# Performance work log

Hardware: AMD Instinct MI355X
Metric: run time of the kernel (lower is better)

Reference implementation:

```python
import jax, jax.numpy as jnp
import numpy as np

D = 2048  # dims
T = 8192  # sequence length


def _layernorm(x, g, b):
    m = jnp.mean(x, axis=-1, keepdims=True)
    v = jnp.mean(jnp.square(x - m), axis=-1, keepdims=True)
    return (x - m) * jax.lax.rsqrt(v + 1e-5) * g + b


def _lerp(a, b, t):
    # torch.lerp(a, b, t) = a + t*(b-a)
    return a + t * (b - a)


def _wkv(k, v, time_first, time_decay):
    """RWKV power-decay attention (numerically stable scan).
    k, v: [T, D]. w = -exp(time_decay) is the per-channel log-decay."""
    u = time_first
    w = -jnp.exp(time_decay)

    def step(carry, kv):
        aa, bb, pp = carry  # running num, den, max-exponent, each [D]
        kt, vt = kv
        ww = u + kt
        p = jnp.maximum(pp, ww)
        e1 = jnp.exp(pp - p)
        e2 = jnp.exp(ww - p)
        out = (e1 * aa + e2 * vt) / (e1 * bb + e2)
        ww2 = pp + w
        p2 = jnp.maximum(ww2, kt)
        e1 = jnp.exp(ww2 - p2)
        e2 = jnp.exp(kt - p2)
        return (e1 * aa + e2 * vt, e1 * bb + e2, p2), out

    init = (jnp.zeros((D,), k.dtype), jnp.zeros((D,), k.dtype),
            jnp.full((D,), -1e38, k.dtype))
    _, out = jax.lax.scan(step, init, (k, v))
    return out  # [T, D]


def setup_inputs() -> dict:
    key = jax.random.key(0)
    ks = iter(jax.random.split(key, 40))
    s = 1.0 / np.sqrt(D)
    inp = {"x": jax.random.normal(next(ks), (T, D), jnp.float32)}
    for name in ["attk", "attv", "attr", "atto", "ffnk", "ffnv", "ffnr"]:
        inp[name + "_w"] = jax.random.normal(next(ks), (D, D), jnp.float32) * s
        inp[name + "_b"] = jax.random.normal(next(ks), (D,), jnp.float32) * 0.02
    inp["ln1_g"] = jnp.ones((D,), jnp.float32)
    inp["ln1_b"] = jnp.zeros((D,), jnp.float32)
    inp["ln2_g"] = jnp.ones((D,), jnp.float32)
    inp["ln2_b"] = jnp.zeros((D,), jnp.float32)
    for name in ["attmixk", "attmixv", "attmixr", "ffnmixk", "ffnmixr"]:
        inp[name] = jax.random.uniform(next(ks), (D,), jnp.float32)
    inp["time_first"] = jax.random.normal(next(ks), (D,), jnp.float32) * 0.1
    inp["time_decay"] = jax.random.normal(next(ks), (D,), jnp.float32) * 0.1
    return inp


def reference(x, attk_w, attk_b, attv_w, attv_b, attr_w, attr_b, atto_w, atto_b,
              ffnk_w, ffnk_b, ffnv_w, ffnv_b, ffnr_w, ffnr_b,
              ln1_g, ln1_b, ln2_g, ln2_b,
              attmixk, attmixv, attmixr, ffnmixk, ffnmixr,
              time_first, time_decay):
    # --- time-mix (attention) branch ---
    xy = _layernorm(x, ln1_g, ln1_b)
    tc = jnp.roll(xy, 1, axis=0)  # token shift
    k = _lerp(tc, xy, attmixk) @ attk_w.T + attk_b
    v = _lerp(tc, xy, attmixv) @ attv_w.T + attv_b
    r = jax.nn.sigmoid(_lerp(tc, xy, attmixr) @ attr_w.T + attr_b)
    wkv = _wkv(k, v, time_first, time_decay) * r
    rz = x + wkv @ atto_w.T + atto_b
    # --- channel-mix (FFN) branch ---
    ddd = _layernorm(rz, ln2_g, ln2_b)
    rc = jnp.roll(ddd, 1, axis=0)
    rf = jax.nn.sigmoid(_lerp(rc, ddd, ffnmixr) @ ffnr_w.T + ffnr_b)
    kf = jax.nn.relu(_lerp(rc, ddd, ffnmixk) @ ffnk_w.T + ffnk_b)
    rvm = jnp.square(kf) @ ffnv_w.T + ffnv_b
    return rvm * rf + rz
```

## Files before the change

### kernel.cpp

```cpp
#include <hip/hip_runtime.h>
#include <cstdint>
#include <cstddef>


#define SEQ 8192
#define DIM 2048
#define NCH 128
#define CL  64

typedef unsigned short u16;
typedef __attribute__((ext_vector_type(8))) short bf16x8;
typedef __attribute__((ext_vector_type(4))) float f32x4;

__device__ __forceinline__ u16 f2bf(float f) {
  unsigned x = __float_as_uint(f);
  x += 0x7fffu + ((x >> 16) & 1u);
  return (u16)(x >> 16);
}
__device__ __forceinline__ float bf2f(u16 h) {
  return __uint_as_float((unsigned)h << 16);
}

__global__ void __launch_bounds__(256) convert_weights(
    const float* w0, const float* w1, const float* w2, const float* w3,
    const float* w4, const float* w5, const float* w6, u16* dst)
{
  const float* s;
  switch (blockIdx.y) {
    case 0: s = w0; break; case 1: s = w1; break; case 2: s = w2; break;
    case 3: s = w3; break; case 4: s = w4; break; case 5: s = w5; break;
    default: s = w6; break;
  }
  size_t i = ((size_t)blockIdx.x * 256 + threadIdx.x) * 4;
  float4 f = *(const float4*)(s + i);
  *(ushort4*)(dst + (size_t)blockIdx.y * DIM * DIM + i) =
      make_ushort4(f2bf(f.x), f2bf(f.y), f2bf(f.z), f2bf(f.w));
}

__device__ __forceinline__ void store_mix8(u16* dst, const float* mix,
                                           const float* yc, const float* yp)
{
  float4 ma = *(const float4*)(mix);
  float4 mb = *(const float4*)(mix + 4);
  float mv[8] = {ma.x, ma.y, ma.z, ma.w, mb.x, mb.y, mb.z, mb.w};
  u16 uu[8];
  #pragma unroll
  for (int j = 0; j < 8; ++j)
    uu[j] = f2bf(yp[j] + mv[j] * (yc[j] - yp[j]));
  *(ushort4*)dst       = make_ushort4(uu[0], uu[1], uu[2], uu[3]);
  *(ushort4*)(dst + 4) = make_ushort4(uu[4], uu[5], uu[6], uu[7]);
}

template<int NOUT>
__global__ void __launch_bounds__(256) ln_mix_kernel(
    const float* __restrict__ X, const float* __restrict__ gw, const float* __restrict__ bw,
    const float* __restrict__ mix0, const float* __restrict__ mix1, const float* __restrict__ mix2,
    u16* __restrict__ o0, u16* __restrict__ o1, u16* __restrict__ o2)
{
  const int t  = blockIdx.x;
  const int tp = (t == 0) ? (SEQ - 1) : (t - 1);
  const int tid = threadIdx.x, lane = tid & 63, wid = tid >> 6;
  const int base = tid * 8;
  const float* xc = X + (size_t)t  * DIM + base;
  const float* xp = X + (size_t)tp * DIM + base;
  float4 ca = *(const float4*)xc, cb2 = *(const float4*)(xc + 4);
  float4 pa = *(const float4*)xp, pb2 = *(const float4*)(xp + 4);
  float cv[8] = {ca.x, ca.y, ca.z, ca.w, cb2.x, cb2.y, cb2.z, cb2.w};
  float pv[8] = {pa.x, pa.y, pa.z, pa.w, pb2.x, pb2.y, pb2.z, pb2.w};
  float4 s = {0.f, 0.f, 0.f, 0.f};
  #pragma unroll
  for (int j = 0; j < 8; ++j) {
    s.x += cv[j]; s.y += cv[j] * cv[j];
    s.z += pv[j]; s.w += pv[j] * pv[j];
  }
  #pragma unroll
  for (int off = 32; off > 0; off >>= 1) {
    s.x += __shfl_down(s.x, off);
    s.y += __shfl_down(s.y, off);
    s.z += __shfl_down(s.z, off);
    s.w += __shfl_down(s.w, off);
  }
  __shared__ float4 wred[4];
  if (lane == 0) wred[wid] = s;
  __syncthreads();
  float4 tt;
  tt.x = wred[0].x + wred[1].x + wred[2].x + wred[3].x;
  tt.y = wred[0].y + wred[1].y + wred[2].y + wred[3].y;
  tt.z = wred[0].z + wred[1].z + wred[2].z + wred[3].z;
  tt.w = wred[0].w + wred[1].w + wred[2].w + wred[3].w;
  constexpr float inv = 1.0f / DIM;
  const float mc = tt.x * inv, vc = tt.y * inv - mc * mc;
  const float rc = 1.0f / sqrtf(vc + 1e-5f);
  const float mp = tt.z * inv, vp = tt.w * inv - mp * mp;
  const float rp = 1.0f / sqrtf(vp + 1e-5f);
  float4 ga = *(const float4*)(gw + base), gb = *(const float4*)(gw + base + 4);
  float4 ba = *(const float4*)(bw + base), bb = *(const float4*)(bw + base + 4);
  float gv[8] = {ga.x, ga.y, ga.z, ga.w, gb.x, gb.y, gb.z, gb.w};
  float bv[8] = {ba.x, ba.y, ba.z, ba.w, bb.x, bb.y, bb.z, bb.w};
  float yc[8], yp[8];
  #pragma unroll
  for (int j = 0; j < 8; ++j) {
    yc[j] = (cv[j] - mc) * rc * gv[j] + bv[j];
    yp[j] = (pv[j] - mp) * rp * gv[j] + bv[j];
  }
  store_mix8(o0 + (size_t)t * DIM + base, mix0 + base, yc, yp);
  store_mix8(o1 + (size_t)t * DIM + base, mix1 + base, yc, yp);
  if constexpr (NOUT == 3)
    store_mix8(o2 + (size_t)t * DIM + base, mix2 + base, yc, yp);
}

template<int EPI>
__global__ void __launch_bounds__(256, 4) gemm_bt(
    const u16* __restrict__ A, const u16* __restrict__ B,
    const float* __restrict__ bias,
    const float* __restrict__ exf, const u16* __restrict__ exb,
    float* __restrict__ Cf, u16* __restrict__ Cb)
{
  constexpr int BK = 32;
  constexpr int NT = DIM / BK;
  __shared__ u16 As[2][128 * BK];
  __shared__ u16 Bs[2][128 * BK];
  const int tid  = threadIdx.x;
  const int lane = tid & 63;
  const int wid  = tid >> 6;
  const int wr = wid >> 1, wc = wid & 1;
  const int bid = blockIdx.y * gridDim.x + blockIdx.x;
  const int nb  = (bid & 7) * 128 + (bid >> 3);
  const int tn  = (nb & 15) * 128;
  const int tm  = (nb >> 4) * 128;
  const int frow = lane & 15, fko = (lane >> 4) * 8;
  const int cb = wid * 2;
  f32x4 acc[4][4] = {};

#define GSTAGE(b, k0)                                                           \
  {                                                                             \
    _Pragma("unroll")                                                           \
    for (int j = 0; j < 2; ++j) {                                               \
      const int chunk = (cb + j) * 64 + lane;                                   \
      const int row = chunk >> 2;                                               \
      const int c8  = (chunk & 3) * 8;                                          \
      const u16* ga = A + (size_t)(tm + row) * DIM + (k0) + c8;                 \
      const u16* gb = B + (size_t)(tn + row) * DIM + (k0) + c8;                 \
      __builtin_amdgcn_global_load_lds(                                         \
          (const __attribute__((address_space(1))) void*)ga,                    \
          (__attribute__((address_space(3))) void*)(&As[b][0] + (cb + j) * 512),\
          16, 0, 0);                                                            \
      __builtin_amdgcn_global_load_lds(                                         \
          (const __attribute__((address_space(1))) void*)gb,                    \
          (__attribute__((address_space(3))) void*)(&Bs[b][0] + (cb + j) * 512),\
          16, 0, 0);                                                            \
    }                                                                           \
  }

#define GCOMPUTE(b)                                                             \
  {                                                                             \
    bf16x8 af[4], bfr[4];                                                       \
    _Pragma("unroll")                                                           \
    for (int m = 0; m < 4; ++m)                                                 \
      af[m] = *(const bf16x8*)(&As[b][0] + (wr * 64 + m * 16 + frow) * BK + fko);\
    _Pragma("unroll")                                                           \
    for (int n = 0; n < 4; ++n)                                                 \
      bfr[n] = *(const bf16x8*)(&Bs[b][0] + (wc * 64 + n * 16 + frow) * BK + fko);\
    _Pragma("unroll")                                                           \
    for (int m = 0; m < 4; ++m)                                                 \
      _Pragma("unroll")                                                         \
      for (int n = 0; n < 4; ++n)                                               \
        acc[m][n] = __builtin_amdgcn_mfma_f32_16x16x32_bf16(af[m], bfr[n],      \
                                                            acc[m][n], 0, 0, 0);\
  }

  GSTAGE(0, 0);
  __syncthreads();
  #pragma unroll 1
  for (int t = 0; t < NT; t += 2) {
    GSTAGE(1, (t + 1) * BK);
    GCOMPUTE(0);
    __syncthreads();
    if (t + 2 < NT) GSTAGE(0, (t + 2) * BK);
    GCOMPUTE(1);
    __syncthreads();
  }
#undef GSTAGE
#undef GCOMPUTE

  #pragma unroll
  for (int n = 0; n < 4; ++n) {
    const int cn = tn + wc * 64 + n * 16 + frow;
    const float bv = bias[cn];
    #pragma unroll
    for (int m = 0; m < 4; ++m) {
      const int r0 = tm + wr * 64 + m * 16 + (lane >> 4) * 4;
      #pragma unroll
      for (int i = 0; i < 4; ++i) {
        const size_t idx = (size_t)(r0 + i) * DIM + cn;
        float val = acc[m][n][i] + bv;
        if constexpr (EPI == 0)      { Cb[idx] = f2bf(val); }
        else if constexpr (EPI == 1) { Cb[idx] = f2bf(1.0f / (1.0f + __expf(-val))); }
        else if constexpr (EPI == 2) { Cf[idx] = val + exf[idx]; }
        else if constexpr (EPI == 3) { float r = fmaxf(val, 0.0f); Cb[idx] = f2bf(r * r); }
        else                         { Cf[idx] = val * bf2f(exb[idx]) + exf[idx]; }
      }
    }
  }
}

__global__ void __launch_bounds__(256) wkv_phase1(
    const u16* __restrict__ k, const u16* __restrict__ v,
    const float* __restrict__ tdec,
    float* __restrict__ Sa, float* __restrict__ Sb, float* __restrict__ Sp)
{
  const int d = blockIdx.y * 256 + threadIdx.x;
  const int c = blockIdx.x;
  const float w = -__expf(tdec[d]);
  float aa = 0.f, bb = 0.f, pp = -1e38f;
  const int t0 = c * CL;
  for (int t = t0; t < t0 + CL; ++t) {
    const size_t idx = (size_t)t * DIM + d;
    const float kk = bf2f(k[idx]), vv = bf2f(v[idx]);
    const float ww2 = pp + w;
    const float p2 = fmaxf(ww2, kk);
    const float e1 = __expf(ww2 - p2), e2 = __expf(kk - p2);
    aa = e1 * aa + e2 * vv;
    bb = e1 * bb + e2;
    pp = p2;
  }
  Sa[(size_t)c * DIM + d] = aa;
  Sb[(size_t)c * DIM + d] = bb;
  Sp[(size_t)c * DIM + d] = pp;
}

__global__ void __launch_bounds__(256) wkv_phase2(
    const float* __restrict__ Sa, const float* __restrict__ Sb, const float* __restrict__ Sp,
    const float* __restrict__ tdec,
    float* __restrict__ Pa, float* __restrict__ Pb, float* __restrict__ Pp)
{
  const int d = blockIdx.x * 256 + threadIdx.x;
  const float w = -__expf(tdec[d]);
  const float Lw = (float)CL * w;
  float aa = 0.f, bb = 0.f, pp = -1e38f;
  for (int c = 0; c < NCH; ++c) {
    const size_t idx = (size_t)c * DIM + d;
    Pa[idx] = aa; Pb[idx] = bb; Pp[idx] = pp;
    const float dp = pp + Lw;
    const float sa = Sa[idx], sb = Sb[idx], sp = Sp[idx];
    const float p = fmaxf(dp, sp);
    const float e1 = __expf(dp - p), e2 = __expf(sp - p);
    aa = e1 * aa + e2 * sa;
    bb = e1 * bb + e2 * sb;
    pp = p;
  }
}

__global__ void __launch_bounds__(256) wkv_phase3(
    const u16* __restrict__ k, const u16* __restrict__ v, const u16* __restrict__ r,
    const float* __restrict__ Pa, const float* __restrict__ Pb, const float* __restrict__ Pp,
    const float* __restrict__ tfirst, const float* __restrict__ tdec,
    u16* __restrict__ outb)
{
  const int d = blockIdx.y * 256 + threadIdx.x;
  const int c = blockIdx.x;
  const float u = tfirst[d];
  const float w = -__expf(tdec[d]);
  const size_t sidx = (size_t)c * DIM + d;
  float aa = Pa[sidx], bb = Pb[sidx], pp = Pp[sidx];
  const int t0 = c * CL;
  for (int t = t0; t < t0 + CL; ++t) {
    const size_t idx = (size_t)t * DIM + d;
    const float kk = bf2f(k[idx]), vv = bf2f(v[idx]);
    const float ww = u + kk;
    const float p = fmaxf(pp, ww);
    float e1 = __expf(pp - p), e2 = __expf(ww - p);
    const float out = (e1 * aa + e2 * vv) / (e1 * bb + e2);
    outb[idx] = f2bf(out * bf2f(r[idx]));
    const float ww2 = pp + w;
    const float p2 = fmaxf(ww2, kk);
    e1 = __expf(ww2 - p2); e2 = __expf(kk - p2);
    aa = e1 * aa + e2 * vv;
    bb = e1 * bb + e2;
    pp = p2;
  }
}

extern "C" void kernel_launch(void* const* d_in, const int* in_sizes, int n_in,
                              void* d_out, int out_size, void* d_ws, size_t ws_size,
                              hipStream_t stream)
{
  const float* x      = (const float*)d_in[0];
  const float* attk_w = (const float*)d_in[1];
  const float* attk_b = (const float*)d_in[2];
  const float* attv_w = (const float*)d_in[3];
  const float* attv_b = (const float*)d_in[4];
  const float* attr_w = (const float*)d_in[5];
  const float* attr_b = (const float*)d_in[6];
  const float* atto_w = (const float*)d_in[7];
  const float* atto_b = (const float*)d_in[8];
  const float* ffnk_w = (const float*)d_in[9];
  const float* ffnk_b = (const float*)d_in[10];
  const float* ffnv_w = (const float*)d_in[11];
  const float* ffnv_b = (const float*)d_in[12];
  const float* ffnr_w = (const float*)d_in[13];
  const float* ffnr_b = (const float*)d_in[14];
  const float* ln1_g  = (const float*)d_in[15];
  const float* ln1_b  = (const float*)d_in[16];
  const float* ln2_g  = (const float*)d_in[17];
  const float* ln2_b  = (const float*)d_in[18];
  const float* amixk  = (const float*)d_in[19];
  const float* amixv  = (const float*)d_in[20];
  const float* amixr  = (const float*)d_in[21];
  const float* fmixk  = (const float*)d_in[22];
  const float* fmixr  = (const float*)d_in[23];
  const float* tfirst = (const float*)d_in[24];
  const float* tdecay = (const float*)d_in[25];
  float* out = (float*)d_out;

  const size_t WE = (size_t)DIM * DIM;
  const size_t SD = (size_t)SEQ * DIM;
  u16* Wbf = (u16*)d_ws;
  u16* xk  = Wbf + 7 * WE;
  u16* xv  = xk + SD;
  u16* xr  = xv + SD;
  u16* kb  = xr + SD;
  u16* vb  = kb + SD;
  u16* rb  = vb + SD;
  float* Sa = (float*)(rb + SD);
  float* Sb = Sa + (size_t)NCH * DIM;
  float* Sp = Sb + (size_t)NCH * DIM;
  float* Pa = Sp + (size_t)NCH * DIM;
  float* Pb = Pa + (size_t)NCH * DIM;
  float* Pp = Pb + (size_t)NCH * DIM;
  u16*   wkvr = xk;
  float* rz   = (float*)xv;
  u16*   xkf  = kb;
  u16*   xrf  = vb;
  u16*   rf   = rb;
  u16*   kf2  = xk;

  const dim3 gg(DIM / 128, SEQ / 128);
  const dim3 gwkv(NCH, DIM / 256);

  convert_weights<<<dim3(DIM * DIM / 1024, 7), 256, 0, stream>>>(
      attk_w, attv_w, attr_w, atto_w, ffnk_w, ffnv_w, ffnr_w, Wbf);

  ln_mix_kernel<3><<<SEQ, 256, 0, stream>>>(x, ln1_g, ln1_b, amixk, amixv, amixr, xk, xv, xr);
  gemm_bt<0><<<gg, 256, 0, stream>>>(xk, Wbf + 0 * WE, attk_b, nullptr, nullptr, nullptr, kb);
  gemm_bt<0><<<gg, 256, 0, stream>>>(xv, Wbf + 1 * WE, attv_b, nullptr, nullptr, nullptr, vb);
  gemm_bt<1><<<gg, 256, 0, stream>>>(xr, Wbf + 2 * WE, attr_b, nullptr, nullptr, nullptr, rb);
  wkv_phase1<<<gwkv, 256, 0, stream>>>(kb, vb, tdecay, Sa, Sb, Sp);
  wkv_phase2<<<DIM / 256, 256, 0, stream>>>(Sa, Sb, Sp, tdecay, Pa, Pb, Pp);
  wkv_phase3<<<gwkv, 256, 0, stream>>>(kb, vb, rb, Pa, Pb, Pp, tfirst, tdecay, wkvr);
  gemm_bt<2><<<gg, 256, 0, stream>>>(wkvr, Wbf + 3 * WE, atto_b, x, nullptr, rz, nullptr);

  ln_mix_kernel<2><<<SEQ, 256, 0, stream>>>(rz, ln2_g, ln2_b, fmixk, fmixr, nullptr, xkf, xrf, nullptr);
  gemm_bt<1><<<gg, 256, 0, stream>>>(xrf, Wbf + 6 * WE, ffnr_b, nullptr, nullptr, nullptr, rf);
  gemm_bt<3><<<gg, 256, 0, stream>>>(xkf, Wbf + 4 * WE, ffnk_b, nullptr, nullptr, nullptr, kf2);
  gemm_bt<4><<<gg, 256, 0, stream>>>(kf2, Wbf + 5 * WE, ffnv_b, rz, rf, out, nullptr);
}
```

Measured before the change: 1.006 ms.

## Use 256x256 GEMM tiles with 4-stage LDS pipeline and swizzled layout

Rewrites the bf16 GEMM to use 256x256 output tiles computed by 512 threads (8 waves, 128x64 per wave), with a 4-buffer LDS ring prefetching three k-steps ahead and gated by vmcnt waits. The LDS layout is XOR-swizzled to reduce bank conflicts on fragment reads, and MFMA sections get raised wave priority. The larger tile is meant to raise arithmetic intensity and hide global-load latency. In exchange it uses much more LDS (128KB) and registers, and launches only 256 blocks, which may leave CUs underused or lower occupancy.

After: 1.124 ms. 1.12x slower.

```diff
diff --git a/kernel.cpp b/kernel.cpp
--- a/kernel.cpp
+++ b/kernel.cpp
@@ -110,7 +110,7 @@
 }
 
 template<int EPI>
-__global__ void __launch_bounds__(256, 4) gemm_bt(
+__global__ void __launch_bounds__(512, 2) gemm_bt(
     const u16* __restrict__ A, const u16* __restrict__ B,
     const float* __restrict__ bias,
     const float* __restrict__ exf, const u16* __restrict__ exb,
@@ -118,78 +118,103 @@
 {
   constexpr int BK = 32;
   constexpr int NT = DIM / BK;
-  __shared__ u16 As[2][128 * BK];
-  __shared__ u16 Bs[2][128 * BK];
+  __shared__ u16 As[4][256 * BK];
+  __shared__ u16 Bs[4][256 * BK];
   const int tid  = threadIdx.x;
   const int lane = tid & 63;
   const int wid  = tid >> 6;
-  const int wr = wid >> 1, wc = wid & 1;
-  const int bid = blockIdx.y * gridDim.x + blockIdx.x;
-  const int nb  = (bid & 7) * 128 + (bid >> 3);
-  const int tn  = (nb & 15) * 128;
-  const int tm  = (nb >> 4) * 128;
-  const int frow = lane & 15, fko = (lane >> 4) * 8;
-  const int cb = wid * 2;
-  f32x4 acc[4][4] = {};
-
-#define GSTAGE(b, k0)                                                           \
+  const int wr   = wid >> 2;
+  const int wc   = wid & 3;
+  const int bid = blockIdx.x;
+  const int nb  = (bid & 7) * 32 + (bid >> 3);
+  const int tm  = (nb >> 3) * 256;
+  const int tn  = (nb & 7) * 256;
+  const int frow = lane & 15;
+  const int fkc  = lane >> 4;
+
+  f32x4 acc[8][4] = {};
+
+#define STAGE(b, kt)                                                            \
   {                                                                             \
+    const int k0 = (kt) * BK;                                                   \
     _Pragma("unroll")                                                           \
     for (int j = 0; j < 2; ++j) {                                               \
-      const int chunk = (cb + j) * 64 + lane;                                   \
-      const int row = chunk >> 2;                                               \
-      const int c8  = (chunk & 3) * 8;                                          \
-      const u16* ga = A + (size_t)(tm + row) * DIM + (k0) + c8;                 \
-      const u16* gb = B + (size_t)(tn + row) * DIM + (k0) + c8;                 \
+      const int p   = (j * 512 + tid) * 16;                                     \
+      const int q   = p ^ (((p >> 7) & 3) << 4);                                \
+      const int row = q >> 6;                                                   \
+      const int ce  = (q & 63) >> 1;                                            \
       __builtin_amdgcn_global_load_lds(                                         \
-          (const __attribute__((address_space(1))) void*)ga,                    \
-          (__attribute__((address_space(3))) void*)(&As[b][0] + (cb + j) * 512),\
-          16, 0, 0);                                                            \
-      __builtin_amdgcn_global_load_lds(                                         \
-          (const __attribute__((address_space(1))) void*)gb,                    \
-          (__attribute__((address_space(3))) void*)(&Bs[b][0] + (cb + j) * 512),\
+          (const __attribute__((address_space(1))) void*)                       \
+              (A + (size_t)(tm + row) * DIM + k0 + ce),                         \
+          (__attribute__((address_space(3))) void*)((char*)&As[b][0] + p),      \
           16, 0, 0);                                                            \
     }                                                                           \
-  }
-
-#define GCOMPUTE(b)                                                             \
+    _Pragma("unroll")                                                           \
+    for (int j = 0; j < 2; ++j) {                                               \
+      const int p   = (j * 512 + tid) * 16;                                     \
+      const int q   = p ^ (((p >> 7) & 3) << 4);                                \
+      const int row = q >> 6;                                                   \
+      const int ce  = (q & 63) >> 1;                                            \
+      __builtin_amdgcn_global_load_lds(                                         \
+          (const __attribute__((address_space(1))) void*)                       \
+              (B + (size_t)(tn + row) * DIM + k0 + ce),                         \
+          (__attribute__((address_space(3))) void*)((char*)&Bs[b][0] + p),      \
+          16, 0, 0);                                                            \
+    }                                                                           \
+  }
+
+#define COMPUTE(b)                                                              \
   {                                                                             \
-    bf16x8 af[4], bfr[4];                                                       \
-    _Pragma("unroll")                                                           \
-    for (int m = 0; m < 4; ++m)                                                 \
-      af[m] = *(const bf16x8*)(&As[b][0] + (wr * 64 + m * 16 + frow) * BK + fko);\
-    _Pragma("unroll")                                                           \
-    for (int n = 0; n < 4; ++n)                                                 \
-      bfr[n] = *(const bf16x8*)(&Bs[b][0] + (wc * 64 + n * 16 + frow) * BK + fko);\
-    _Pragma("unroll")                                                           \
-    for (int m = 0; m < 4; ++m)                                                 \
+    bf16x8 af[8], bfr[4];                                                       \
+    _Pragma("unroll")                                                           \
+    for (int m = 0; m < 8; ++m) {                                               \
+      const int row = wr * 128 + m * 16 + frow;                                 \
+      const int off = row * 64 + ((fkc ^ ((row >> 1) & 3)) * 16);               \
+      af[m] = *(const bf16x8*)((const char*)&As[b][0] + off);                   \
+    }                                                                           \
+    _Pragma("unroll")                                                           \
+    for (int n = 0; n < 4; ++n) {                                               \
+      const int row = wc * 64 + n * 16 + frow;                                  \
+      const int off = row * 64 + ((fkc ^ ((row >> 1) & 3)) * 16);               \
+      bfr[n] = *(const bf16x8*)((const char*)&Bs[b][0] + off);                  \
+    }                                                                           \
+    __builtin_amdgcn_s_setprio(1);                                              \
+    _Pragma("unroll")                                                           \
+    for (int m = 0; m < 8; ++m)                                                 \
       _Pragma("unroll")                                                         \
       for (int n = 0; n < 4; ++n)                                               \
         acc[m][n] = __builtin_amdgcn_mfma_f32_16x16x32_bf16(af[m], bfr[n],      \
                                                             acc[m][n], 0, 0, 0);\
-  }
-
-  GSTAGE(0, 0);
-  __syncthreads();
+    __builtin_amdgcn_s_setprio(0);                                              \
+  }
+
+  STAGE(0, 0); STAGE(1, 1); STAGE(2, 2);
   #pragma unroll 1
-  for (int t = 0; t < NT; t += 2) {
-    GSTAGE(1, (t + 1) * BK);
-    GCOMPUTE(0);
-    __syncthreads();
-    if (t + 2 < NT) GSTAGE(0, (t + 2) * BK);
-    GCOMPUTE(1);
-    __syncthreads();
-  }
-#undef GSTAGE
-#undef GCOMPUTE
+  for (int t = 0; t < NT - 2; ++t) {
+    asm volatile("s_waitcnt vmcnt(8)" ::: "memory");
+    __builtin_amdgcn_s_barrier();
+    __builtin_amdgcn_sched_barrier(0);
+    if (t < NT - 3) STAGE((t + 3) & 3, t + 3);
+    COMPUTE(t & 3);
+  }
+  asm volatile("s_waitcnt vmcnt(4)" ::: "memory");
+  __builtin_amdgcn_s_barrier();
+  __builtin_amdgcn_sched_barrier(0);
+  COMPUTE((NT - 2) & 3);
+  asm volatile("s_waitcnt vmcnt(0)" ::: "memory");
+  __builtin_amdgcn_s_barrier();
+  __builtin_amdgcn_sched_barrier(0);
+  COMPUTE((NT - 1) & 3);
+#undef STAGE
+#undef COMPUTE
 
   #pragma unroll
   for (int n = 0; n < 4; ++n) {
     const int cn = tn + wc * 64 + n * 16 + frow;
     const float bv = bias[cn];
     #pragma unroll
-    for (int m = 0; m < 4; ++m) {
-      const int r0 = tm + wr * 64 + m * 16 + (lane >> 4) * 4;
+    for (int m = 0; m < 8; ++m) {
+      const int r0 = tm + wr * 128 + m * 16 + (lane >> 4) * 4;
       #pragma unroll
       for (int i = 0; i < 4; ++i) {
         const size_t idx = (size_t)(r0 + i) * DIM + cn;
@@ -335,23 +360,23 @@
   u16*   rf   = rb;
   u16*   kf2  = xk;
 
-  const dim3 gg(DIM / 128, SEQ / 128);
+  const dim3 gg(256);
   const dim3 gwkv(NCH, DIM / 256);
 
   convert_weights<<<dim3(DIM * DIM / 1024, 7), 256, 0, stream>>>(
       attk_w, attv_w, attr_w, atto_w, ffnk_w, ffnv_w, ffnr_w, Wbf);
 
   ln_mix_kernel<3><<<SEQ, 256, 0, stream>>>(x, ln1_g, ln1_b, amixk, amixv, amixr, xk, xv, xr);
-  gemm_bt<0><<<gg, 256, 0, stream>>>(xk, Wbf + 0 * WE, attk_b, nullptr, nullptr, nullptr, kb);
-  gemm_bt<0><<<gg, 256, 0, stream>>>(xv, Wbf + 1 * WE, attv_b, nullptr, nullptr, nullptr, vb);
-  gemm_bt<1><<<gg, 256, 0, stream>>>(xr, Wbf + 2 * WE, attr_b, nullptr, nullptr, nullptr, rb);
+  gemm_bt<0><<<gg, 512, 0, stream>>>(xk, Wbf + 0 * WE, attk_b, nullptr, nullptr, nullptr, kb);
+  gemm_bt<0><<<gg, 512, 0, stream>>>(xv, Wbf + 1 * WE, attv_b, nullptr, nullptr, nullptr, vb);
+  gemm_bt<1><<<gg, 512, 0, stream>>>(xr, Wbf + 2 * WE, attr_b, nullptr, nullptr, nullptr, rb);
   wkv_phase1<<<gwkv, 256, 0, stream>>>(kb, vb, tdecay, Sa, Sb, Sp);
   wkv_phase2<<<DIM / 256, 256, 0, stream>>>(Sa, Sb, Sp, tdecay, Pa, Pb, Pp);
   wkv_phase3<<<gwkv, 256, 0, stream>>>(kb, vb, rb, Pa, Pb, Pp, tfirst, tdecay, wkvr);
-  gemm_bt<2><<<gg, 256, 0, stream>>>(wkvr, Wbf + 3 * WE, atto_b, x, nullptr, rz, nullptr);
+  gemm_bt<2><<<gg, 512, 0, stream>>>(wkvr, Wbf + 3 * WE, atto_b, x, nullptr, rz, nullptr);
 
   ln_mix_kernel<2><<<SEQ, 256, 0, stream>>>(rz, ln2_g, ln2_b, fmixk, fmixr, nullptr, xkf, xrf, nullptr);
-  gemm_bt<1><<<gg, 256, 0, stream>>>(xrf, Wbf + 6 * WE, ffnr_b, nullptr, nullptr, nullptr, rf);
-  gemm_bt<3><<<gg, 256, 0, stream>>>(xkf, Wbf + 4 * WE, ffnk_b, nullptr, nullptr, nullptr, kf2);
-  gemm_bt<4><<<gg, 256, 0, stream>>>(kf2, Wbf + 5 * WE, ffnv_b, rz, rf, out, nullptr);
-}
+  gemm_bt<1><<<gg, 512, 0, stream>>>(xrf, Wbf + 6 * WE, ffnr_b, nullptr, nullptr, nullptr, rf);
+  gemm_bt<3><<<gg, 512, 0, stream>>>(xkf, Wbf + 4 * WE, ffnk_b, nullptr, nullptr, nullptr, kf2);
+  gemm_bt<4><<<gg, 512, 0, stream>>>(kf2, Wbf + 5 * WE, ffnv_b, rz, rf, out, nullptr);
+}
```
